# Optimization experiments

Measured on AMD Instinct MI355X. Metric: run time of the kernel, lower is better.

## Reference

```python
import jax, jax.numpy as jnp
import numpy as np

KERNEL_SIZE = 5
SIGMA_SPATIAL = 1.0
SIGMA_RANGE = 0.1
EPS = 1e-8


def _spatial_kernel(k: int, sigma: float) -> jnp.ndarray:
    coords = jnp.arange(k, dtype=jnp.float32) - (k - 1) / 2.0
    d2 = coords[:, None] ** 2 + coords[None, :] ** 2
    return jnp.exp(-d2 / (2.0 * sigma ** 2))


def setup_inputs() -> dict:
    key = jax.random.key(0)
    x = jax.random.uniform(key, (4, 3, 512, 512), dtype=jnp.float32)
    spatial_kernel = _spatial_kernel(KERNEL_SIZE, SIGMA_SPATIAL)
    return {"x": x, "spatial_kernel": spatial_kernel}


def reference(x, spatial_kernel):
    # x: (B, C, H, W); spatial_kernel: (k, k)
    k = KERNEL_SIZE
    p = k // 2
    B, C, H, W = x.shape
    xp = jnp.pad(x, ((0, 0), (0, 0), (p, p), (p, p)), mode="reflect")
    # Stack the k*k shifted windows -> (B, C, H, W, k*k). This is the
    # vectorized equivalent of the per-pixel patch extraction.
    patches = jnp.stack(
        [xp[:, :, di:di + H, dj:dj + W] for di in range(k) for dj in range(k)],
        axis=-1,
    )
    center = x[..., None]  # (B, C, H, W, 1)
    range_w = jnp.exp(-((patches - center) ** 2) / (2.0 * SIGMA_RANGE ** 2))
    weights = range_w * spatial_kernel.reshape(-1)  # broadcast over last axis
    weights_norm = weights / (jnp.sum(weights, axis=-1, keepdims=True) + EPS)
    return jnp.sum(patches * weights_norm, axis=-1)  # (B, C, H, W)
```

## Files before the change

### kernel.cpp

```cpp
#include <hip/hip_runtime.h>

#define IMG_H 512
#define IMG_W 512

#define LOG2E 1.4426950408889634f
#define HALF_LOG2E 0.7213475204444817f

#define EXP2_SCALE 8388608.0f
#define EXP2_BIAS 1065055989.0f

typedef float v2f __attribute__((ext_vector_type(2)));

static __device__ __forceinline__ v2f pk_fma(v2f a, v2f b, v2f c) {
  v2f d;
  asm("v_pk_fma_f32 %0, %1, %2, %3" : "=v"(d) : "v"(a), "v"(b), "v"(c));
  return d;
}
static __device__ __forceinline__ v2f pk_nfma(v2f a, v2f b, v2f c) {
  v2f d;
  asm("v_pk_fma_f32 %0, %1, %2, %3 neg_lo:[1,0,0] neg_hi:[1,0,0]"
      : "=v"(d) : "v"(a), "v"(b), "v"(c));
  return d;
}
static __device__ __forceinline__ v2f pk_add(v2f a, v2f b) {
  v2f d;
  asm("v_pk_add_f32 %0, %1, %2" : "=v"(d) : "v"(a), "v"(b));
  return d;
}

static __device__ __forceinline__ float fast_rcp(float x) {
  return __builtin_amdgcn_rcpf(x);
}

static __device__ __forceinline__ void load_row2(const float* __restrict__ rowp,
                                                 int t, int li, int ri,
                                                 bool le, bool re, float win[6]) {
  const float2* __restrict__ rp = (const float2*)rowp;
  float2 L = rp[li];
  float2 C = rp[t];
  float2 R = rp[ri];
  win[0] = le ? R.x : L.x;
  win[1] = le ? C.y : L.y;
  win[2] = C.x;
  win[3] = C.y;
  win[4] = re ? C.x : R.x;
  win[5] = re ? L.y : R.y;
}

template <int DI>
static __device__ __forceinline__ void row_accum2(const float win[6], v2f A2,
                                                  v2f nca2, v2f& ws2, v2f& vs2) {
#pragma unroll
  for (int dj = 0; dj < 5; ++dj) {
    const int d2s = (DI - 2) * (DI - 2) + (dj - 2) * (dj - 2);
    const float lsk = -HALF_LOG2E * (float)d2s;
    const v2f lsk2 = {lsk, lsk};
    v2f val = {win[dj], win[dj + 1]};
    v2f da = pk_fma(val, A2, nca2);
    v2f e = pk_nfma(da, da, lsk2);
    v2f tt = pk_fma(e, (v2f){EXP2_SCALE, EXP2_SCALE},
                    (v2f){EXP2_BIAS, EXP2_BIAS});
    unsigned u0 = (unsigned)tt.x;
    unsigned u1 = (unsigned)tt.y;
    v2f rw;
    rw.x = __uint_as_float(u0);
    rw.y = __uint_as_float(u1);
    ws2 = pk_add(ws2, rw);
    vs2 = pk_fma(rw, val, vs2);
  }
}

__global__ __launch_bounds__(256) void bilateral_kernel(
    const float* __restrict__ x, float* __restrict__ out) {
  const int t  = blockIdx.x * 64 + threadIdx.x;
  const int hy = blockIdx.y * 4 + threadIdx.y;
  const int plane = blockIdx.z;

  const size_t pbase = (size_t)plane * (IMG_H * IMG_W);
  const float* __restrict__ img = x + pbase;

  const int li = (t > 0) ? t - 1 : 0;
  const int ri = (t < IMG_W / 2 - 1) ? t + 1 : IMG_W / 2 - 1;
  const bool le = (t == 0);
  const bool re = (t == IMG_W / 2 - 1);

  int r0 = hy - 2; r0 = (r0 < 0) ? -r0 : r0;
  int r1 = hy - 1; r1 = (r1 < 0) ? -r1 : r1;
  int r3 = hy + 1; r3 = (r3 >= IMG_H) ? (2 * IMG_H - 2 - r3) : r3;
  int r4 = hy + 2; r4 = (r4 >= IMG_H) ? (2 * IMG_H - 2 - r4) : r4;

  const float A = sqrtf(50.0f * LOG2E);
  const v2f A2 = {A, A};

  v2f ws2 = {0.f, 0.f};
  v2f vs2 = {0.f, 0.f};

  float w2[6];
  load_row2(img + (size_t)hy * IMG_W, t, li, ri, le, re, w2);
  const v2f nca2 = {-w2[2] * A, -w2[3] * A};
  row_accum2<2>(w2, A2, nca2, ws2, vs2);

  float win[6];
  load_row2(img + (size_t)r0 * IMG_W, t, li, ri, le, re, win);
  row_accum2<0>(win, A2, nca2, ws2, vs2);
  load_row2(img + (size_t)r1 * IMG_W, t, li, ri, le, re, win);
  row_accum2<1>(win, A2, nca2, ws2, vs2);
  load_row2(img + (size_t)r3 * IMG_W, t, li, ri, le, re, win);
  row_accum2<3>(win, A2, nca2, ws2, vs2);
  load_row2(img + (size_t)r4 * IMG_W, t, li, ri, le, re, win);
  row_accum2<4>(win, A2, nca2, ws2, vs2);

  float2 res;
  res.x = vs2.x * fast_rcp(ws2.x);
  res.y = vs2.y * fast_rcp(ws2.y);

  float2* __restrict__ op = (float2*)(out + pbase + (size_t)hy * IMG_W);
  op[t] = res;
}

extern "C" void kernel_launch(void* const* d_in, const int* in_sizes, int n_in,
                              void* d_out, int out_size, void* d_ws, size_t ws_size,
                              hipStream_t stream) {
  const float* x = (const float*)d_in[0];
  float* out = (float*)d_out;

  const int planes = in_sizes[0] / (IMG_H * IMG_W);

  dim3 block(64, 4, 1);
  dim3 grid(IMG_W / 128, IMG_H / 4, planes);
  bilateral_kernel<<<grid, block, 0, stream>>>(x, out);
}
```

Before: 20.92 us.

## Compute two output rows per thread and specialize interior blocks without edge handling

```diff
diff --git a/kernel.cpp b/kernel.cpp
--- a/kernel.cpp
+++ b/kernel.cpp
@@ -27,95 +27,101 @@
   asm("v_pk_add_f32 %0, %1, %2" : "=v"(d) : "v"(a), "v"(b));
   return d;
 }
-
 static __device__ __forceinline__ float fast_rcp(float x) {
   return __builtin_amdgcn_rcpf(x);
 }
 
-static __device__ __forceinline__ void load_row2(const float* __restrict__ rowp,
-                                                 int t, int li, int ri,
-                                                 bool le, bool re, float win[6]) {
-  const float2* __restrict__ rp = (const float2*)rowp;
-  float2 L = rp[li];
-  float2 C = rp[t];
-  float2 R = rp[ri];
-  win[0] = le ? R.x : L.x;
-  win[1] = le ? C.y : L.y;
-  win[2] = C.x;
-  win[3] = C.y;
-  win[4] = re ? C.x : R.x;
-  win[5] = re ? L.y : R.y;
-}
-
-template <int DI>
-static __device__ __forceinline__ void row_accum2(const float win[6], v2f A2,
-                                                  v2f nca2, v2f& ws2, v2f& vs2) {
-#pragma unroll
-  for (int dj = 0; dj < 5; ++dj) {
-    const int d2s = (DI - 2) * (DI - 2) + (dj - 2) * (dj - 2);
-    const float lsk = -HALF_LOG2E * (float)d2s;
-    const v2f lsk2 = {lsk, lsk};
-    v2f val = {win[dj], win[dj + 1]};
-    v2f da = pk_fma(val, A2, nca2);
-    v2f e = pk_nfma(da, da, lsk2);
-    v2f tt = pk_fma(e, (v2f){EXP2_SCALE, EXP2_SCALE},
-                    (v2f){EXP2_BIAS, EXP2_BIAS});
-    unsigned u0 = (unsigned)tt.x;
-    unsigned u1 = (unsigned)tt.y;
-    v2f rw;
-    rw.x = __uint_as_float(u0);
-    rw.y = __uint_as_float(u1);
-    ws2 = pk_add(ws2, rw);
-    vs2 = pk_fma(rw, val, vs2);
-  }
-}
-
 __global__ __launch_bounds__(256) void bilateral_kernel(
     const float* __restrict__ x, float* __restrict__ out) {
-  const int t  = blockIdx.x * 64 + threadIdx.x;
-  const int hy = blockIdx.y * 4 + threadIdx.y;
+  const int t   = blockIdx.x * 64 + threadIdx.x;
+  const int rp  = blockIdx.y * 4 + threadIdx.y;
+  const int hy0 = rp * 2;
   const int plane = blockIdx.z;
 
   const size_t pbase = (size_t)plane * (IMG_H * IMG_W);
   const float* __restrict__ img = x + pbase;
 
-  const int li = (t > 0) ? t - 1 : 0;
-  const int ri = (t < IMG_W / 2 - 1) ? t + 1 : IMG_W / 2 - 1;
-  const bool le = (t == 0);
-  const bool re = (t == IMG_W / 2 - 1);
+  int rows[6];
+#pragma unroll
+  for (int k = 0; k < 6; ++k) {
+    int r = hy0 + k - 2;
+    r = (r < 0) ? -r : ((r >= IMG_H) ? (2 * IMG_H - 2 - r) : r);
+    rows[k] = r;
+  }
 
-  int r0 = hy - 2; r0 = (r0 < 0) ? -r0 : r0;
-  int r1 = hy - 1; r1 = (r1 < 0) ? -r1 : r1;
-  int r3 = hy + 1; r3 = (r3 >= IMG_H) ? (2 * IMG_H - 2 - r3) : r3;
-  int r4 = hy + 2; r4 = (r4 >= IMG_H) ? (2 * IMG_H - 2 - r4) : r4;
+  float win[6][6];
+
+  const bool edgeBlock = (blockIdx.x == 0) | (blockIdx.x == gridDim.x - 1);
+  if (!edgeBlock) {
+#pragma unroll
+    for (int k = 0; k < 6; ++k) {
+      const float2* __restrict__ r2 = (const float2*)(img + (size_t)rows[k] * IMG_W);
+      float2 L = r2[t - 1], C = r2[t], R = r2[t + 1];
+      win[k][0] = L.x; win[k][1] = L.y;
+      win[k][2] = C.x; win[k][3] = C.y;
+      win[k][4] = R.x; win[k][5] = R.y;
+    }
+  } else {
+    const int li = (t > 0) ? t - 1 : 0;
+    const int ri = (t < IMG_W / 2 - 1) ? t + 1 : IMG_W / 2 - 1;
+    const bool le = (t == 0);
+    const bool re = (t == IMG_W / 2 - 1);
+#pragma unroll
+    for (int k = 0; k < 6; ++k) {
+      const float2* __restrict__ r2 = (const float2*)(img + (size_t)rows[k] * IMG_W);
+      float2 L = r2[li], C = r2[t], R = r2[ri];
+      win[k][0] = le ? R.x : L.x;
+      win[k][1] = le ? C.y : L.y;
+      win[k][2] = C.x; win[k][3] = C.y;
+      win[k][4] = re ? C.x : R.x;
+      win[k][5] = re ? L.y : R.y;
+    }
+  }
 
   const float A = sqrtf(50.0f * LOG2E);
   const v2f A2 = {A, A};
 
-  v2f ws2 = {0.f, 0.f};
-  v2f vs2 = {0.f, 0.f};
+  v2f ws[2] = {{0.f, 0.f}, {0.f, 0.f}};
+  v2f vs[2] = {{0.f, 0.f}, {0.f, 0.f}};
+  v2f nca[2];
+#pragma unroll
+  for (int p = 0; p < 2; ++p) {
+    nca[p].x = -win[p + 2][2] * A;
+    nca[p].y = -win[p + 2][3] * A;
+  }
 
-  float w2[6];
-  load_row2(img + (size_t)hy * IMG_W, t, li, ri, le, re, w2);
-  const v2f nca2 = {-w2[2] * A, -w2[3] * A};
-  row_accum2<2>(w2, A2, nca2, ws2, vs2);
+#pragma unroll
+  for (int di = 0; di < 5; ++di) {
+#pragma unroll
+    for (int dj = 0; dj < 5; ++dj) {
+      const int d2s = (di - 2) * (di - 2) + (dj - 2) * (dj - 2);
+      const float lsk = -HALF_LOG2E * (float)d2s;
+      const v2f lsk2 = {lsk, lsk};
+#pragma unroll
+      for (int p = 0; p < 2; ++p) {
+        v2f val = {win[p + di][dj], win[p + di][dj + 1]};
+        v2f da = pk_fma(val, A2, nca[p]);
+        v2f e = pk_nfma(da, da, lsk2);
+        v2f tt = pk_fma(e, (v2f){EXP2_SCALE, EXP2_SCALE},
+                        (v2f){EXP2_BIAS, EXP2_BIAS});
+        v2f rw;
+        rw.x = __uint_as_float((unsigned)tt.x);
+        rw.y = __uint_as_float((unsigned)tt.y);
+        ws[p] = pk_add(ws[p], rw);
+        vs[p] = pk_fma(rw, val, vs[p]);
+      }
+    }
+  }
 
-  float win[6];
-  load_row2(img + (size_t)r0 * IMG_W, t, li, ri, le, re, win);
-  row_accum2<0>(win, A2, nca2, ws2, vs2);
-  load_row2(img + (size_t)r1 * IMG_W, t, li, ri, le, re, win);
-  row_accum2<1>(win, A2, nca2, ws2, vs2);
-  load_row2(img + (size_t)r3 * IMG_W, t, li, ri, le, re, win);
-  row_accum2<3>(win, A2, nca2, ws2, vs2);
-  load_row2(img + (size_t)r4 * IMG_W, t, li, ri, le, re, win);
-  row_accum2<4>(win, A2, nca2, ws2, vs2);
-
-  float2 res;
-  res.x = vs2.x * fast_rcp(ws2.x);
-  res.y = vs2.y * fast_rcp(ws2.y);
-
-  float2* __restrict__ op = (float2*)(out + pbase + (size_t)hy * IMG_W);
-  op[t] = res;
+#pragma unroll
+  for (int p = 0; p < 2; ++p) {
+    float2 res;
+    res.x = vs[p].x * fast_rcp(ws[p].x);
+    res.y = vs[p].y * fast_rcp(ws[p].y);
+    float2* __restrict__ op =
+        (float2*)(out + pbase + (size_t)(hy0 + p) * IMG_W);
+    op[t] = res;
+  }
 }
 
 extern "C" void kernel_launch(void* const* d_in, const int* in_sizes, int n_in,
@@ -127,6 +133,6 @@
   const int planes = in_sizes[0] / (IMG_H * IMG_W);
 
   dim3 block(64, 4, 1);
-  dim3 grid(IMG_W / 128, IMG_H / 4, planes);
+  dim3 grid(IMG_W / 128, IMG_H / 8, planes);
   bilateral_kernel<<<grid, block, 0, stream>>>(x, out);
 }
```

After: 19.16 us. -8.4%, faster.
